# Optimization experiments

Measured on AMD Instinct MI355X. Metric: run time of the kernel, lower is better.

## Reference

```python
import jax, jax.numpy as jnp
import numpy as np

N_SRC = 50000      # columns of adj / rows of x
N_SAMP = 50000     # rows of adj (sampled nodes this layer)
N_TOTAL = 200000   # rows of historical embedding buffer
E = 1600000        # nnz of adj
D_IN = 256
D_OUT = 256


def setup_inputs() -> dict:
    key = jax.random.key(0)
    ks = jax.random.split(key, 10)
    x = jax.random.normal(ks[0], (N_SRC, D_IN), dtype=jnp.float32)
    adj_row = jax.random.randint(ks[1], (E,), 0, N_SAMP, dtype=jnp.int32)
    adj_col = jax.random.randint(ks[2], (E,), 0, N_SRC, dtype=jnp.int32)
    adj_val = jax.random.uniform(ks[3], (E,), dtype=jnp.float32)
    nodes_per_layer = jax.random.randint(ks[4], (N_SAMP,), 0, N_TOTAL, dtype=jnp.int32)
    y_buf = jax.random.normal(ks[5], (N_TOTAL, D_IN), dtype=jnp.float32)
    W = jax.random.normal(ks[6], (D_IN, D_OUT), dtype=jnp.float32) / np.sqrt(D_IN)
    b = jax.random.normal(ks[7], (D_OUT,), dtype=jnp.float32) * 0.01
    scale = jnp.ones((D_OUT,), dtype=jnp.float32)
    offset = jnp.zeros((D_OUT,), dtype=jnp.float32)
    return {"x": x, "adj_row": adj_row, "adj_col": adj_col, "adj_val": adj_val,
            "nodes_per_layer": nodes_per_layer, "y_buf": y_buf,
            "W": W, "b": b, "scale": scale, "offset": offset}


def reference(x, adj_row, adj_col, adj_val, nodes_per_layer, y_buf, W, b, scale, offset):
    # ---- sparse aggregation: feat = spmm(adj, x)  [N_SAMP, D_IN]
    msgs = adj_val[:, None] * x[adj_col]                         # [E, D_IN]
    feat = jax.ops.segment_sum(msgs, adj_row, num_segments=N_SAMP)
    # ---- momentum blend with historical embeddings (training path)
    feat = 0.9 * y_buf[nodes_per_layer] + 0.1 * feat
    # buffer update: sampled rows <- feat.detach(); all other rows *= 0.9
    new_y = (y_buf * 0.9).at[nodes_per_layer].set(jax.lax.stop_gradient(feat))
    # ---- linear -> ELU -> custom per-row normalization
    out = jax.nn.elu(feat @ W + b)                               # [N_SAMP, D_OUT]
    mean = out.mean(axis=1, keepdims=True)
    var = out.var(axis=1, keepdims=True) + 1e-9                  # unbiased=False
    out = (out - mean) * scale * jax.lax.rsqrt(var) + offset
    return out, new_y
```

## Files before the change

kernel.cpp:

```cpp
#include <hip/hip_runtime.h>
#include <math.h>

#define N_SRC   50000
#define N_SAMP  50000
#define N_TOTAL 200000
#define NE      1600000
#define D       256

#define CBSHIFT 12
#define NB      13
#define NCELL   (N_SAMP * NB)

typedef float f32x4 __attribute__((ext_vector_type(4)));

__device__ __forceinline__ float4 ntload4(const float* p) {
    f32x4 t = __builtin_nontemporal_load((const f32x4*)p);
    return make_float4(t.x, t.y, t.z, t.w);
}
__device__ __forceinline__ void ntstore4(float* p, float4 v) {
    f32x4 t; t.x = v.x; t.y = v.y; t.z = v.z; t.w = v.w;
    __builtin_nontemporal_store(t, (f32x4*)p);
}

__global__ __launch_bounds__(256) void k_init(
    int* __restrict__ cellcnt, int* __restrict__ owner, int* __restrict__ gtotal)
{
    int i = blockIdx.x * 256 + threadIdx.x;
    if (i < NCELL)   cellcnt[i] = 0;
    if (i < N_TOTAL) owner[i]   = -1;
    if (i == 0)      *gtotal    = 0;
}

__global__ __launch_bounds__(256) void k_count(
    const int* __restrict__ adj_row, const int* __restrict__ adj_col,
    const int* __restrict__ nodes, int* __restrict__ cellcnt, int* __restrict__ owner)
{
    int idx = blockIdx.x * 256 + threadIdx.x;
    if (idx < NE) {
        int row = adj_row[idx];
        int col = adj_col[idx];
        atomicAdd(&cellcnt[row * NB + (col >> CBSHIFT)], 1);
    }
    if (idx < N_SAMP) {
        atomicMax(&owner[nodes[idx]], idx);
    }
}

__global__ __launch_bounds__(256) void k_rowalloc(
    const int* __restrict__ cellcnt, int* __restrict__ cellcur,
    int* __restrict__ rowptr, int* __restrict__ rowcnt, int* __restrict__ gtotal)
{
    int r = blockIdx.x * 256 + threadIdx.x;
    if (r >= N_SAMP) return;
    int pref[NB];
    int sum = 0;
    #pragma unroll
    for (int cb = 0; cb < NB; ++cb) {
        pref[cb] = sum;
        sum += cellcnt[r * NB + cb];
    }
    int base = atomicAdd(gtotal, sum);
    rowptr[r] = base;
    rowcnt[r] = sum;
    #pragma unroll
    for (int cb = 0; cb < NB; ++cb)
        cellcur[r * NB + cb] = base + pref[cb];
}

__global__ __launch_bounds__(256) void k_scatter(
    const int* __restrict__ adj_row, const int* __restrict__ adj_col,
    const float* __restrict__ adj_val, int* __restrict__ cellcur, int2* __restrict__ bucket)
{
    int idx = blockIdx.x * 256 + threadIdx.x;
    if (idx >= NE) return;
    int row = adj_row[idx];
    int col = adj_col[idx];
    float val = adj_val[idx];
    int pos = atomicAdd(&cellcur[row * NB + (col >> CBSHIFT)], 1);
    bucket[pos] = make_int2(col, __float_as_int(val));
}

__global__ __launch_bounds__(256) void k_spmm_blend(
    const float* __restrict__ x, const int2* __restrict__ bucket,
    const int* __restrict__ rowptr, const int* __restrict__ rowcnt,
    const int* __restrict__ nodes, const int* __restrict__ owner,
    const float* __restrict__ y_buf, float* __restrict__ feat, float* __restrict__ newy)
{
    int wave = threadIdx.x >> 6;
    int lane = threadIdx.x & 63;
    int row  = blockIdx.x * 4 + wave;
    int off  = lane * 4;

    int cnt = rowcnt[row];
    const int2* bk = bucket + rowptr[row];
    float4 acc = make_float4(0.f, 0.f, 0.f, 0.f);
    int j = 0;
    for (; j + 3 < cnt; j += 4) {
        int2 e0 = bk[j],     e1 = bk[j + 1];
        int2 e2 = bk[j + 2], e3 = bk[j + 3];
        float v0 = __int_as_float(e0.y), v1 = __int_as_float(e1.y);
        float v2 = __int_as_float(e2.y), v3 = __int_as_float(e3.y);
        float4 x0 = *(const float4*)(x + (size_t)e0.x * D + off);
        float4 x1 = *(const float4*)(x + (size_t)e1.x * D + off);
        float4 x2 = *(const float4*)(x + (size_t)e2.x * D + off);
        float4 x3 = *(const float4*)(x + (size_t)e3.x * D + off);
        acc.x += v0 * x0.x + v1 * x1.x + v2 * x2.x + v3 * x3.x;
        acc.y += v0 * x0.y + v1 * x1.y + v2 * x2.y + v3 * x3.y;
        acc.z += v0 * x0.z + v1 * x1.z + v2 * x2.z + v3 * x3.z;
        acc.w += v0 * x0.w + v1 * x1.w + v2 * x2.w + v3 * x3.w;
    }
    for (; j < cnt; ++j) {
        int2 e0 = bk[j];
        float v0 = __int_as_float(e0.y);
        float4 x0 = *(const float4*)(x + (size_t)e0.x * D + off);
        acc.x += v0 * x0.x; acc.y += v0 * x0.y;
        acc.z += v0 * x0.z; acc.w += v0 * x0.w;
    }
    int node = nodes[row];
    float4 yv = ntload4(y_buf + (size_t)node * D + off);
    float4 f;
    f.x = 0.9f * yv.x + 0.1f * acc.x;
    f.y = 0.9f * yv.y + 0.1f * acc.y;
    f.z = 0.9f * yv.z + 0.1f * acc.z;
    f.w = 0.9f * yv.w + 0.1f * acc.w;
    *(float4*)(feat + (size_t)row * D + off) = f;
    if (owner[node] == row)
        ntstore4(newy + (size_t)node * D + off, f);

    int base = row * 4;
    int4 ow = *(const int4*)&owner[base];
    #pragma unroll
    for (int k = 0; k < 4; ++k) {
        int o = (k == 0) ? ow.x : (k == 1) ? ow.y : (k == 2) ? ow.z : ow.w;
        if (o < 0) {
            int r = base + k;
            float4 y = ntload4(y_buf + (size_t)r * D + off);
            ntstore4(newy + (size_t)r * D + off,
                     make_float4(0.9f * y.x, 0.9f * y.y, 0.9f * y.z, 0.9f * y.w));
        }
    }
}

__global__ __launch_bounds__(256) void k_gemm_elu_norm(
    float* __restrict__ io, const float* __restrict__ Wm,
    const float* __restrict__ b, const float* __restrict__ scale,
    const float* __restrict__ offset)
{
    __shared__ float ldsF[32][256];
    __shared__ float ldsW[32][256];
    int t    = threadIdx.x;
    int quad = t >> 6;
    int lane = t & 63;
    int r0   = blockIdx.x * 32;

    #pragma unroll
    for (int p = 0; p < 8; ++p) {
        int m  = p * 4 + quad;
        int c4 = lane * 4;
        int r  = r0 + m;
        float4 v = (r < N_SAMP) ? ntload4(io + (size_t)r * D + c4)
                                : make_float4(0.f, 0.f, 0.f, 0.f);
        *(float4*)&ldsF[m][c4] = v;
    }

    int m0 = quad * 8;
    int c0 = lane * 4;
    float acc[8][4];
    #pragma unroll
    for (int mm = 0; mm < 8; ++mm)
        for (int i = 0; i < 4; ++i) acc[mm][i] = 0.f;

    for (int kt = 0; kt < 256; kt += 32) {
        __syncthreads();
        #pragma unroll
        for (int p = 0; p < 8; ++p) {
            int kk = p * 4 + quad;
            int c4 = lane * 4;
            *(float4*)&ldsW[kk][c4] = *(const float4*)(Wm + (size_t)(kt + kk) * D + c4);
        }
        __syncthreads();
        #pragma unroll
        for (int k = 0; k < 32; ++k) {
            float4 wv = *(float4*)&ldsW[k][c0];
            #pragma unroll
            for (int mm = 0; mm < 8; ++mm) {
                float fm = ldsF[m0 + mm][kt + k];
                acc[mm][0] += fm * wv.x;
                acc[mm][1] += fm * wv.y;
                acc[mm][2] += fm * wv.z;
                acc[mm][3] += fm * wv.w;
            }
        }
    }

    float4 bv = *(const float4*)(b + c0);
    float4 sv = *(const float4*)(scale + c0);
    float4 ov = *(const float4*)(offset + c0);

    #pragma unroll
    for (int mm = 0; mm < 8; ++mm) {
        float o0 = acc[mm][0] + bv.x;
        float o1 = acc[mm][1] + bv.y;
        float o2 = acc[mm][2] + bv.z;
        float o3 = acc[mm][3] + bv.w;
        o0 = o0 > 0.f ? o0 : expf(o0) - 1.f;
        o1 = o1 > 0.f ? o1 : expf(o1) - 1.f;
        o2 = o2 > 0.f ? o2 : expf(o2) - 1.f;
        o3 = o3 > 0.f ? o3 : expf(o3) - 1.f;
        float s = o0 + o1 + o2 + o3;
        float q = o0 * o0 + o1 * o1 + o2 * o2 + o3 * o3;
        #pragma unroll
        for (int d2 = 1; d2 < 64; d2 <<= 1) {
            s += __shfl_xor(s, d2, 64);
            q += __shfl_xor(q, d2, 64);
        }
        float mean = s * (1.0f / 256.0f);
        float var  = q * (1.0f / 256.0f) - mean * mean + 1e-9f;
        float rstd = rsqrtf(var);
        int r = r0 + m0 + mm;
        if (r < N_SAMP) {
            float4 res;
            res.x = (o0 - mean) * sv.x * rstd + ov.x;
            res.y = (o1 - mean) * sv.y * rstd + ov.y;
            res.z = (o2 - mean) * sv.z * rstd + ov.z;
            res.w = (o3 - mean) * sv.w * rstd + ov.w;
            ntstore4(io + (size_t)r * D + c0, res);
        }
    }
}

extern "C" void kernel_launch(void* const* d_in, const int* in_sizes, int n_in,
                              void* d_out, int out_size, void* d_ws, size_t ws_size,
                              hipStream_t stream) {
    const float* x       = (const float*)d_in[0];
    const int*   adj_row = (const int*)  d_in[1];
    const int*   adj_col = (const int*)  d_in[2];
    const float* adj_val = (const float*)d_in[3];
    const int*   nodes   = (const int*)  d_in[4];
    const float* y_buf   = (const float*)d_in[5];
    const float* Wm      = (const float*)d_in[6];
    const float* b       = (const float*)d_in[7];
    const float* scale   = (const float*)d_in[8];
    const float* offset  = (const float*)d_in[9];

    float* out  = (float*)d_out;
    float* newy = out + (size_t)N_SAMP * D;

    char* ws      = (char*)d_ws;
    int*  cellcnt = (int*)(ws);
    int*  cellcur = (int*)(ws + 3  * 1024 * 1024);
    int*  rowptr  = (int*)(ws + 6  * 1024 * 1024);
    int*  rowcnt  = (int*)(ws + 6  * 1024 * 1024 + 256 * 1024);
    int*  gtotal  = (int*)(ws + 6  * 1024 * 1024 + 512 * 1024);
    int*  owner   = (int*)(ws + 7  * 1024 * 1024);
    int2* bucket  = (int2*)(ws + 8 * 1024 * 1024);

    k_init    <<<(NCELL + 255) / 256,  256, 0, stream>>>(cellcnt, owner, gtotal);
    k_count   <<<(NE + 255) / 256,     256, 0, stream>>>(adj_row, adj_col, nodes, cellcnt, owner);
    k_rowalloc<<<(N_SAMP + 255) / 256, 256, 0, stream>>>(cellcnt, cellcur, rowptr, rowcnt, gtotal);
    k_scatter <<<(NE + 255) / 256,     256, 0, stream>>>(adj_row, adj_col, adj_val, cellcur, bucket);
    k_spmm_blend<<<N_SAMP / 4, 256, 0, stream>>>(
        x, bucket, rowptr, rowcnt, nodes, owner, y_buf, out, newy);
    k_gemm_elu_norm<<<(N_SAMP + 31) / 32, 256, 0, stream>>>(out, Wm, b, scale, offset);
}
```

Before: 975.9 us.

## Gather x in fp16 for SpMM and use split-bf16 MFMA for the GEMM

Adds a prep kernel that converts x to fp16, so the SpMM gather reads half as many bytes per edge. It also replaces the scalar FP32 GEMM with MFMA bf16 16x16x32 instructions, using a hi/lo bf16 split (three products per tile) to keep close to FP32 accuracy. The row norm reduction is redone with cross-wave LDS partial sums. The risks are fp16 rounding error in the aggregation, plus the extra conversion passes over x and W.

```diff
diff --git a/kernel.cpp b/kernel.cpp
--- a/kernel.cpp
+++ b/kernel.cpp
@@ -1,4 +1,5 @@
 #include <hip/hip_runtime.h>
+#include <hip/hip_fp16.h>
 #include <math.h>
 
 #define N_SRC   50000
@@ -11,15 +12,36 @@
 #define NB      13
 #define NCELL   (N_SAMP * NB)
 
-typedef float f32x4 __attribute__((ext_vector_type(4)));
+typedef unsigned short ushort;
+typedef unsigned int   uint;
+using bf16x8 = __attribute__((ext_vector_type(8))) short;
+using f32x4v = __attribute__((ext_vector_type(4))) float;
 
 __device__ __forceinline__ float4 ntload4(const float* p) {
-    f32x4 t = __builtin_nontemporal_load((const f32x4*)p);
+    f32x4v t = __builtin_nontemporal_load((const f32x4v*)p);
     return make_float4(t.x, t.y, t.z, t.w);
 }
 __device__ __forceinline__ void ntstore4(float* p, float4 v) {
-    f32x4 t; t.x = v.x; t.y = v.y; t.z = v.z; t.w = v.w;
-    __builtin_nontemporal_store(t, (f32x4*)p);
+    f32x4v t; t.x = v.x; t.y = v.y; t.z = v.z; t.w = v.w;
+    __builtin_nontemporal_store(t, (f32x4v*)p);
+}
+
+__device__ __forceinline__ ushort bf16_rne(float f) {
+    uint u = __float_as_uint(f);
+    uint r = u + 0x7FFFu + ((u >> 16) & 1u);
+    return (ushort)(r >> 16);
+}
+__device__ __forceinline__ float bf16_tof(ushort h) {
+    return __uint_as_float(((uint)h) << 16);
+}
+
+__device__ __forceinline__ float4 xload4h(const __half* p) {
+    int2 r = *(const int2*)p;
+    __half2 h0 = *(__half2*)&r.x;
+    __half2 h1 = *(__half2*)&r.y;
+    float2 f0 = __half22float2(h0);
+    float2 f1 = __half22float2(h1);
+    return make_float4(f0.x, f0.y, f1.x, f1.y);
 }
 
 __global__ __launch_bounds__(256) void k_init(
@@ -29,6 +51,36 @@
     if (i < NCELL)   cellcnt[i] = 0;
     if (i < N_TOTAL) owner[i]   = -1;
     if (i == 0)      *gtotal    = 0;
+}
+
+__global__ __launch_bounds__(256) void k_prep(
+    const float* __restrict__ x, __half* __restrict__ xh)
+{
+    int i = blockIdx.x * 256 + threadIdx.x;
+    if (i >= (N_SRC * D) / 8) return;
+    const float4* p = (const float4*)x + (size_t)i * 2;
+    float4 a = p[0], c = p[1];
+    __half2 h0 = __floats2half2_rn(a.x, a.y);
+    __half2 h1 = __floats2half2_rn(a.z, a.w);
+    __half2 h2 = __floats2half2_rn(c.x, c.y);
+    __half2 h3 = __floats2half2_rn(c.z, c.w);
+    int4 w;
+    w.x = *(int*)&h0; w.y = *(int*)&h1; w.z = *(int*)&h2; w.w = *(int*)&h3;
+    *(int4*)(xh + (size_t)i * 8) = w;
+}
+
+__global__ __launch_bounds__(256) void k_wsplit(
+    const float* __restrict__ W, ushort* __restrict__ Wt_hi, ushort* __restrict__ Wt_lo)
+{
+    int idx = blockIdx.x * 256 + threadIdx.x;
+    if (idx >= D * D) return;
+    int k = idx >> 8;
+    int n = idx & 255;
+    float f = W[idx];
+    ushort h = bf16_rne(f);
+    ushort l = bf16_rne(f - bf16_tof(h));
+    Wt_hi[n * D + k] = h;
+    Wt_lo[n * D + k] = l;
 }
 
 __global__ __launch_bounds__(256) void k_count(
@@ -81,7 +133,7 @@
 }
 
 __global__ __launch_bounds__(256) void k_spmm_blend(
-    const float* __restrict__ x, const int2* __restrict__ bucket,
+    const __half* __restrict__ xh, const int2* __restrict__ bucket,
     const int* __restrict__ rowptr, const int* __restrict__ rowcnt,
     const int* __restrict__ nodes, const int* __restrict__ owner,
     const float* __restrict__ y_buf, float* __restrict__ feat, float* __restrict__ newy)
@@ -100,10 +152,10 @@
         int2 e2 = bk[j + 2], e3 = bk[j + 3];
         float v0 = __int_as_float(e0.y), v1 = __int_as_float(e1.y);
         float v2 = __int_as_float(e2.y), v3 = __int_as_float(e3.y);
-        float4 x0 = *(const float4*)(x + (size_t)e0.x * D + off);
-        float4 x1 = *(const float4*)(x + (size_t)e1.x * D + off);
-        float4 x2 = *(const float4*)(x + (size_t)e2.x * D + off);
-        float4 x3 = *(const float4*)(x + (size_t)e3.x * D + off);
+        float4 x0 = xload4h(xh + (size_t)e0.x * D + off);
+        float4 x1 = xload4h(xh + (size_t)e1.x * D + off);
+        float4 x2 = xload4h(xh + (size_t)e2.x * D + off);
+        float4 x3 = xload4h(xh + (size_t)e3.x * D + off);
         acc.x += v0 * x0.x + v1 * x1.x + v2 * x2.x + v3 * x3.x;
         acc.y += v0 * x0.y + v1 * x1.y + v2 * x2.y + v3 * x3.y;
         acc.z += v0 * x0.z + v1 * x1.z + v2 * x2.z + v3 * x3.z;
@@ -112,7 +164,7 @@
     for (; j < cnt; ++j) {
         int2 e0 = bk[j];
         float v0 = __int_as_float(e0.y);
-        float4 x0 = *(const float4*)(x + (size_t)e0.x * D + off);
+        float4 x0 = xload4h(xh + (size_t)e0.x * D + off);
         acc.x += v0 * x0.x; acc.y += v0 * x0.y;
         acc.z += v0 * x0.z; acc.w += v0 * x0.w;
     }
@@ -142,89 +194,128 @@
 }
 
 __global__ __launch_bounds__(256) void k_gemm_elu_norm(
-    float* __restrict__ io, const float* __restrict__ Wm,
-    const float* __restrict__ b, const float* __restrict__ scale,
-    const float* __restrict__ offset)
-{
-    __shared__ float ldsF[32][256];
-    __shared__ float ldsW[32][256];
-    int t    = threadIdx.x;
-    int quad = t >> 6;
-    int lane = t & 63;
+    float* __restrict__ io, const ushort* __restrict__ Wt_hi,
+    const ushort* __restrict__ Wt_lo, const float* __restrict__ b,
+    const float* __restrict__ scale, const float* __restrict__ offset)
+{
+    __shared__ ushort Fhi[32][264], Flo[32][264];
+    __shared__ ushort Wh[256][40],  Wl[256][40];
+    __shared__ float  red[2][2][16][2];
+
+    int tid  = threadIdx.x;
+    int w    = tid >> 6;
+    int l    = tid & 63;
+    int g    = l >> 4;
+    int c16  = l & 15;
+    int mt   = w & 1;
+    int nh   = w >> 1;
     int r0   = blockIdx.x * 32;
 
-    #pragma unroll
-    for (int p = 0; p < 8; ++p) {
-        int m  = p * 4 + quad;
-        int c4 = lane * 4;
+    {
+        int m  = tid >> 3;
+        int c0 = (tid & 7) * 32;
         int r  = r0 + m;
-        float4 v = (r < N_SAMP) ? ntload4(io + (size_t)r * D + c4)
-                                : make_float4(0.f, 0.f, 0.f, 0.f);
-        *(float4*)&ldsF[m][c4] = v;
-    }
-
-    int m0 = quad * 8;
-    int c0 = lane * 4;
-    float acc[8][4];
-    #pragma unroll
-    for (int mm = 0; mm < 8; ++mm)
-        for (int i = 0; i < 4; ++i) acc[mm][i] = 0.f;
-
-    for (int kt = 0; kt < 256; kt += 32) {
+        #pragma unroll
+        for (int i = 0; i < 8; ++i) {
+            float4 v = (r < N_SAMP) ? ntload4(io + (size_t)r * D + c0 + i * 4)
+                                    : make_float4(0.f, 0.f, 0.f, 0.f);
+            ushort h0 = bf16_rne(v.x), h1 = bf16_rne(v.y);
+            ushort h2 = bf16_rne(v.z), h3 = bf16_rne(v.w);
+            ushort l0 = bf16_rne(v.x - bf16_tof(h0));
+            ushort l1 = bf16_rne(v.y - bf16_tof(h1));
+            ushort l2 = bf16_rne(v.z - bf16_tof(h2));
+            ushort l3 = bf16_rne(v.w - bf16_tof(h3));
+            int c = c0 + i * 4;
+            uint2 ph, pl;
+            ph.x = (uint)h0 | ((uint)h1 << 16); ph.y = (uint)h2 | ((uint)h3 << 16);
+            pl.x = (uint)l0 | ((uint)l1 << 16); pl.y = (uint)l2 | ((uint)l3 << 16);
+            *(uint2*)&Fhi[m][c] = ph;
+            *(uint2*)&Flo[m][c] = pl;
+        }
+    }
+
+    f32x4v acc[8];
+    #pragma unroll
+    for (int t = 0; t < 8; ++t) acc[t] = (f32x4v)(0.f);
+
+    for (int kt8 = 0; kt8 < 8; ++kt8) {
+        int kt = kt8 * 32;
         __syncthreads();
-        #pragma unroll
-        for (int p = 0; p < 8; ++p) {
-            int kk = p * 4 + quad;
-            int c4 = lane * 4;
-            *(float4*)&ldsW[kk][c4] = *(const float4*)(Wm + (size_t)(kt + kk) * D + c4);
+        {
+            int n = tid;
+            const int4* gh = (const int4*)(Wt_hi + (size_t)n * D + kt);
+            const int4* gl = (const int4*)(Wt_lo + (size_t)n * D + kt);
+            #pragma unroll
+            for (int i = 0; i < 4; ++i) {
+                *(int4*)&Wh[n][i * 8] = gh[i];
+                *(int4*)&Wl[n][i * 8] = gl[i];
+            }
         }
         __syncthreads();
-        #pragma unroll
-        for (int k = 0; k < 32; ++k) {
-            float4 wv = *(float4*)&ldsW[k][c0];
+        int arow = mt * 16 + c16;
+        bf16x8 ah = *(const bf16x8*)&Fhi[arow][kt + g * 8];
+        bf16x8 al = *(const bf16x8*)&Flo[arow][kt + g * 8];
+        #pragma unroll
+        for (int t = 0; t < 8; ++t) {
+            int n = nh * 128 + t * 16 + c16;
+            bf16x8 bh = *(const bf16x8*)&Wh[n][g * 8];
+            bf16x8 bl = *(const bf16x8*)&Wl[n][g * 8];
+            acc[t] = __builtin_amdgcn_mfma_f32_16x16x32_bf16(ah, bh, acc[t], 0, 0, 0);
+            acc[t] = __builtin_amdgcn_mfma_f32_16x16x32_bf16(al, bh, acc[t], 0, 0, 0);
+            acc[t] = __builtin_amdgcn_mfma_f32_16x16x32_bf16(ah, bl, acc[t], 0, 0, 0);
+        }
+    }
+
+    float bcol[8], scol[8], ocol[8];
+    #pragma unroll
+    for (int t = 0; t < 8; ++t) {
+        int c = nh * 128 + t * 16 + c16;
+        bcol[t] = b[c]; scol[t] = scale[c]; ocol[t] = offset[c];
+    }
+    float s[4] = {0.f, 0.f, 0.f, 0.f};
+    float q[4] = {0.f, 0.f, 0.f, 0.f};
+    #pragma unroll
+    for (int t = 0; t < 8; ++t) {
+        #pragma unroll
+        for (int j = 0; j < 4; ++j) {
+            float o = acc[t][j] + bcol[t];
+            o = o > 0.f ? o : expf(o) - 1.f;
+            acc[t][j] = o;
+            s[j] += o;
+            q[j] += o * o;
+        }
+    }
+    #pragma unroll
+    for (int j = 0; j < 4; ++j) {
+        #pragma unroll
+        for (int d2 = 1; d2 < 16; d2 <<= 1) {
+            s[j] += __shfl_xor(s[j], d2, 64);
+            q[j] += __shfl_xor(q[j], d2, 64);
+        }
+    }
+    if (c16 == 0) {
+        #pragma unroll
+        for (int j = 0; j < 4; ++j) {
+            red[mt][nh][g * 4 + j][0] = s[j];
+            red[mt][nh][g * 4 + j][1] = q[j];
+        }
+    }
+    __syncthreads();
+    #pragma unroll
+    for (int j = 0; j < 4; ++j) {
+        int rr = g * 4 + j;
+        float S = red[mt][0][rr][0] + red[mt][1][rr][0];
+        float Q = red[mt][0][rr][1] + red[mt][1][rr][1];
+        float mean = S * (1.0f / 256.0f);
+        float var  = Q * (1.0f / 256.0f) - mean * mean + 1e-9f;
+        float rstd = rsqrtf(var);
+        int r = r0 + mt * 16 + rr;
+        if (r < N_SAMP) {
             #pragma unroll
-            for (int mm = 0; mm < 8; ++mm) {
-                float fm = ldsF[m0 + mm][kt + k];
-                acc[mm][0] += fm * wv.x;
-                acc[mm][1] += fm * wv.y;
-                acc[mm][2] += fm * wv.z;
-                acc[mm][3] += fm * wv.w;
+            for (int t = 0; t < 8; ++t) {
+                int c = nh * 128 + t * 16 + c16;
+                io[(size_t)r * D + c] = (acc[t][j] - mean) * scol[t] * rstd + ocol[t];
             }
-        }
-    }
-
-    float4 bv = *(const float4*)(b + c0);
-    float4 sv = *(const float4*)(scale + c0);
-    float4 ov = *(const float4*)(offset + c0);
-
-    #pragma unroll
-    for (int mm = 0; mm < 8; ++mm) {
-        float o0 = acc[mm][0] + bv.x;
-        float o1 = acc[mm][1] + bv.y;
-        float o2 = acc[mm][2] + bv.z;
-        float o3 = acc[mm][3] + bv.w;
-        o0 = o0 > 0.f ? o0 : expf(o0) - 1.f;
-        o1 = o1 > 0.f ? o1 : expf(o1) - 1.f;
-        o2 = o2 > 0.f ? o2 : expf(o2) - 1.f;
-        o3 = o3 > 0.f ? o3 : expf(o3) - 1.f;
-        float s = o0 + o1 + o2 + o3;
-        float q = o0 * o0 + o1 * o1 + o2 * o2 + o3 * o3;
-        #pragma unroll
-        for (int d2 = 1; d2 < 64; d2 <<= 1) {
-            s += __shfl_xor(s, d2, 64);
-            q += __shfl_xor(q, d2, 64);
-        }
-        float mean = s * (1.0f / 256.0f);
-        float var  = q * (1.0f / 256.0f) - mean * mean + 1e-9f;
-        float rstd = rsqrtf(var);
-        int r = r0 + m0 + mm;
-        if (r < N_SAMP) {
-            float4 res;
-            res.x = (o0 - mean) * sv.x * rstd + ov.x;
-            res.y = (o1 - mean) * sv.y * rstd + ov.y;
-            res.z = (o2 - mean) * sv.z * rstd + ov.z;
-            res.w = (o3 - mean) * sv.w * rstd + ov.w;
-            ntstore4(io + (size_t)r * D + c0, res);
         }
     }
 }
@@ -246,20 +337,25 @@
     float* out  = (float*)d_out;
     float* newy = out + (size_t)N_SAMP * D;
 
-    char* ws      = (char*)d_ws;
-    int*  cellcnt = (int*)(ws);
-    int*  cellcur = (int*)(ws + 3  * 1024 * 1024);
-    int*  rowptr  = (int*)(ws + 6  * 1024 * 1024);
-    int*  rowcnt  = (int*)(ws + 6  * 1024 * 1024 + 256 * 1024);
-    int*  gtotal  = (int*)(ws + 6  * 1024 * 1024 + 512 * 1024);
-    int*  owner   = (int*)(ws + 7  * 1024 * 1024);
-    int2* bucket  = (int2*)(ws + 8 * 1024 * 1024);
-
-    k_init    <<<(NCELL + 255) / 256,  256, 0, stream>>>(cellcnt, owner, gtotal);
-    k_count   <<<(NE + 255) / 256,     256, 0, stream>>>(adj_row, adj_col, nodes, cellcnt, owner);
-    k_rowalloc<<<(N_SAMP + 255) / 256, 256, 0, stream>>>(cellcnt, cellcur, rowptr, rowcnt, gtotal);
-    k_scatter <<<(NE + 255) / 256,     256, 0, stream>>>(adj_row, adj_col, adj_val, cellcur, bucket);
+    char*   ws      = (char*)d_ws;
+    int*    cellcnt = (int*)(ws);
+    int*    cellcur = (int*)(ws + 3  * 1024 * 1024);
+    int*    rowptr  = (int*)(ws + 6  * 1024 * 1024);
+    int*    rowcnt  = (int*)(ws + 6  * 1024 * 1024 + 256 * 1024);
+    int*    gtotal  = (int*)(ws + 6  * 1024 * 1024 + 512 * 1024);
+    int*    owner   = (int*)(ws + 7  * 1024 * 1024);
+    ushort* Wt_hi   = (ushort*)(ws + 8 * 1024 * 1024);
+    ushort* Wt_lo   = (ushort*)(ws + 8 * 1024 * 1024 + 256 * 1024);
+    int2*   bucket  = (int2*)(ws + 9 * 1024 * 1024);
+    __half* xh      = (__half*)(ws + 22 * 1024 * 1024);
+
+    k_init    <<<(NCELL + 255) / 256,      256, 0, stream>>>(cellcnt, owner, gtotal);
+    k_prep    <<<(N_SRC * D / 8 + 255) / 256, 256, 0, stream>>>(x, xh);
+    k_wsplit  <<<(D * D + 255) / 256,      256, 0, stream>>>(Wm, Wt_hi, Wt_lo);
+    k_count   <<<(NE + 255) / 256,         256, 0, stream>>>(adj_row, adj_col, nodes, cellcnt, owner);
+    k_rowalloc<<<(N_SAMP + 255) / 256,     256, 0, stream>>>(cellcnt, cellcur, rowptr, rowcnt, gtotal);
+    k_scatter <<<(NE + 255) / 256,         256, 0, stream>>>(adj_row, adj_col, adj_val, cellcur, bucket);
     k_spmm_blend<<<N_SAMP / 4, 256, 0, stream>>>(
-        x, bucket, rowptr, rowcnt, nodes, owner, y_buf, out, newy);
-    k_gemm_elu_norm<<<(N_SAMP + 31) / 32, 256, 0, stream>>>(out, Wm, b, scale, offset);
-}
+        xh, bucket, rowptr, rowcnt, nodes, owner, y_buf, out, newy);
+    k_gemm_elu_norm<<<(N_SAMP + 31) / 32, 256, 0, stream>>>(out, Wt_hi, Wt_lo, b, scale, offset);
+}
```

After: 837.0 us. -14.2%, faster.
